# Kernel tuning notes

Measured on AMD Instinct MI355X. Metric: run time of the kernel, lower is better.

The kernel has to match this reference:

```python
import jax, jax.numpy as jnp
import numpy as np

V, E, T, H, Z = 32000, 512, 64, 1024, 128
B = 64
PAD = 31999


def _lin(x, W, b):
    return x @ W.T + b


def _lstm_cell(x, h, c, Wih, Whh, bih, bhh):
    gates = x @ Wih.T + bih + h @ Whh.T + bhh  # [B,4H], torch gate order i,f,g,o
    i, f, g, o = jnp.split(gates, 4, axis=-1)
    c = jax.nn.sigmoid(f) * c + jax.nn.sigmoid(i) * jnp.tanh(g)
    h = jax.nn.sigmoid(o) * jnp.tanh(c)
    return h, c


def _forward(enc_input, dec_input, length, eps, enc_emb, enc_Wih, enc_Whh, enc_bih, enc_bhh,
             latent_W, latent_b, dec_emb, attn_W, attn_b, combine_W, combine_b,
             dec_Wih, dec_Whh, dec_bih, dec_bhh, pri_W, pri_b, inf_W, inf_b,
             aux_W, aux_b, out_W, out_b):
    # All lengths == T, so the descending sort and pack/pad are identity ops.
    att_mask = enc_input == PAD  # [B,T]
    x_enc = enc_emb[enc_input]   # [B,T,E]

    def enc_step(carry, x):
        h, c = carry
        h, c = _lstm_cell(x, h, c, enc_Wih, enc_Whh, enc_bih, enc_bhh)
        return (h, c), h

    h0 = jnp.zeros((B, H), x_enc.dtype)
    (h_T, c_T), enc_out = jax.lax.scan(enc_step, (h0, h0), jnp.swapaxes(x_enc, 0, 1))
    enc_output = jnp.swapaxes(enc_out, 0, 1)  # [B,T,H]

    mu, logvar = jnp.split(_lin(jnp.concatenate([h_T, c_T], -1), latent_W, latent_b), 2, -1)
    z = mu + jnp.exp(0.5 * logvar) * eps  # [B,Z]

    x_dec = dec_emb[dec_input]  # [B,T+1,E]; dropout off (eval mode)

    def dec_step(carry, inp):
        h, c = carry
        x, t = inp
        pri_mu, pri_lv = jnp.split(_lin(h, pri_W, pri_b), 2, -1)
        scale = _lin(jnp.concatenate([x, h], -1), attn_W, attn_b)  # [B,T]
        scale = jnp.where(att_mask, -jnp.inf, scale)
        attn_w = jax.nn.softmax(scale, -1)
        context = jnp.einsum('bt,bth->bh', attn_w, enc_output)
        inf_mu, inf_lv = jnp.split(_lin(jnp.concatenate([h, context], -1), inf_W, inf_b), 2, -1)
        mask = (length + 1 > t).astype(x.dtype)  # [B]
        kld = 0.5 * jnp.sum(pri_lv - inf_lv + jnp.exp(inf_lv - pri_lv)
                            + (inf_mu - pri_mu) ** 2 / jnp.exp(pri_lv) - 1.0, axis=1) * mask
        z_step = pri_mu  # eval mode (torch: reparameterize(inf_mu, inf_lv) when training)
        aux_mu = _lin(z_step, aux_W, aux_b)
        aux_c = jnp.sum((jax.lax.stop_gradient(context) - aux_mu) ** 2, axis=1)
        u = _lin(jnp.concatenate([x, aux_mu, z_step, z], -1), combine_W, combine_b)
        h, c = _lstm_cell(u, h, c, dec_Wih, dec_Whh, dec_bih, dec_bhh)
        return (h, c), (h, kld, aux_c)

    ts = jnp.arange(T + 1)
    _, (hs, klds, aux_cs) = jax.lax.scan(dec_step, (h0, h0), (jnp.swapaxes(x_dec, 0, 1), ts))
    output = jnp.swapaxes(hs, 0, 1)  # [B,T+1,H]

    logit = output @ out_W.T + out_b  # [B,T+1,V]
    logp = jax.nn.log_softmax(logit, -1)
    return logp, mu, logvar, jnp.sum(klds), jnp.sum(aux_cs)


def setup_inputs() -> dict:
    key = jax.random.key(0)
    ks = jax.random.split(key, 32)
    s = 0.02
    d = {
        'enc_input': jax.random.randint(ks[0], (B, T), 0, V - 1),
        'dec_input': jax.random.randint(ks[1], (B, T + 1), 0, V - 1),
        'length': jnp.full((B,), T, dtype=jnp.int32),
        'eps': jax.random.normal(ks[2], (B, Z), jnp.float32),
        'enc_emb': (jax.random.normal(ks[3], (V, E)) * s).at[PAD].set(0.0),
        'enc_Wih': jax.random.normal(ks[4], (4 * H, E)) * s,
        'enc_Whh': jax.random.normal(ks[5], (4 * H, H)) * s,
        'enc_bih': jax.random.normal(ks[6], (4 * H,)) * s,
        'enc_bhh': jax.random.normal(ks[7], (4 * H,)) * s,
        'latent_W': jax.random.normal(ks[8], (2 * Z, 2 * H)) * s,
        'latent_b': jax.random.normal(ks[9], (2 * Z,)) * s,
        'dec_emb': (jax.random.normal(ks[10], (V, E)) * s).at[PAD].set(0.0),
        'attn_W': jax.random.normal(ks[11], (T, H + E)) * s,
        'attn_b': jax.random.normal(ks[12], (T,)) * s,
        'combine_W': jax.random.normal(ks[13], (H, H + E + 2 * Z)) * s,
        'combine_b': jax.random.normal(ks[14], (H,)) * s,
        'dec_Wih': jax.random.normal(ks[15], (4 * H, H)) * s,
        'dec_Whh': jax.random.normal(ks[16], (4 * H, H)) * s,
        'dec_bih': jax.random.normal(ks[17], (4 * H,)) * s,
        'dec_bhh': jax.random.normal(ks[18], (4 * H,)) * s,
        'pri_W': jax.random.normal(ks[19], (2 * Z, H)) * s,
        'pri_b': jax.random.normal(ks[20], (2 * Z,)) * s,
        'inf_W': jax.random.normal(ks[21], (2 * Z, 2 * H)) * s,
        'inf_b': jax.random.normal(ks[22], (2 * Z,)) * s,
        'aux_W': jax.random.normal(ks[23], (H, Z)) * s,
        'aux_b': jax.random.normal(ks[24], (H,)) * s,
        'out_W': jax.random.normal(ks[25], (V, H)) * s,
        'out_b': jax.random.normal(ks[26], (V,)) * s,
    }
    return d


def reference(enc_input, dec_input, length, eps, enc_emb, enc_Wih, enc_Whh, enc_bih, enc_bhh,
              latent_W, latent_b, dec_emb, attn_W, attn_b, combine_W, combine_b,
              dec_Wih, dec_Whh, dec_bih, dec_bhh, pri_W, pri_b, inf_W, inf_b,
              aux_W, aux_b, out_W, out_b):
    return _forward(enc_input, dec_input, length, eps, enc_emb, enc_Wih, enc_Whh, enc_bih,
                    enc_bhh, latent_W, latent_b, dec_emb, attn_W, attn_b, combine_W, combine_b,
                    dec_Wih, dec_Whh, dec_bih, dec_bhh, pri_W, pri_b, inf_W, inf_b,
                    aux_W, aux_b, out_W, out_b)
```

## Files before the change

kernel.cpp:

```cpp
#include <hip/hip_runtime.h>
#include <hip/hip_bf16.h>
#include <cmath>

typedef unsigned short u16;
typedef __attribute__((ext_vector_type(8))) short short8;
typedef __attribute__((ext_vector_type(4))) float floatx4;

#define DEVI __device__ __forceinline__

constexpr int cV = 32000, cE = 512, cT = 64, cH = 1024, cZ = 128, cB = 64, cPAD = 31999, cTP1 = 65;
constexpr long long LOGP_SZ = 133120000LL;
constexpr long long AMAT_OFF = 130990080LL;
constexpr long long WBOUT_OFF = 38400000LL;
constexpr int SKIP_LO = 1200, SKIP_HI = 1712;

DEVI float b2f(u16 u) { return __uint_as_float(((unsigned)u) << 16); }
DEVI u16 f2b(float f) {
  unsigned u = __float_as_uint(f);
  unsigned r = u + 0x7FFFu + ((u >> 16) & 1u);
  return (u16)(r >> 16);
}
DEVI unsigned pk2(float lo, float hi) {
  __hip_bfloat162 t = __float22bfloat162_rn(make_float2(lo, hi));
  return *reinterpret_cast<unsigned*>(&t);
}
DEVI float sigm(float x) { return 1.f / (1.f + expf(-x)); }

DEVI short8 ldfragW(const float* __restrict__ p) {
  float4 x = *(const float4*)p, y = *(const float4*)(p + 4);
  union { unsigned u[4]; short8 s; } r;
  r.u[0] = pk2(x.x, x.y); r.u[1] = pk2(x.z, x.w);
  r.u[2] = pk2(y.x, y.y); r.u[3] = pk2(y.z, y.w);
  return r.s;
}

template <typename T>
DEVI short8 ldfrag(const T* __restrict__ p) {
  if constexpr (sizeof(T) == 2) return *(const short8*)(p);
  else return ldfragW((const float*)p);
}

template <int MAP>
DEVI int rmap(int r) {
  if constexpr (MAP == 1) return ((r & 3) << 10) | (r >> 2);
  else if constexpr (MAP == 2) return r & 63;
  else return r;
}

DEVI float dot_wf(const float* __restrict__ w, const float* __restrict__ s, int K) {
  float a0 = 0.f, a1 = 0.f, a2 = 0.f, a3 = 0.f;
#pragma unroll 4
  for (int k = 0; k < K; k += 8) {
    float4 p = *(const float4*)(w + k);
    float4 q = *(const float4*)(w + k + 4);
    a0 = fmaf(s[k + 0], p.x, a0); a1 = fmaf(s[k + 1], p.y, a1);
    a2 = fmaf(s[k + 2], p.z, a2); a3 = fmaf(s[k + 3], p.w, a3);
    a0 = fmaf(s[k + 4], q.x, a0); a1 = fmaf(s[k + 5], q.y, a1);
    a2 = fmaf(s[k + 6], q.z, a2); a3 = fmaf(s[k + 7], q.w, a3);
  }
  return (a0 + a1) + (a2 + a3);
}

__global__ __launch_bounds__(256) void k_zero(float* p, int n) {
  int i = blockIdx.x * 256 + threadIdx.x;
  if (i < n) p[i] = 0.f;
}

template <typename AT, typename BT, typename CT, int AMAP, int BMAP, bool ADDC>
__global__ __launch_bounds__(64) void k_gemm(
    const AT* __restrict__ A, int lda, const BT* __restrict__ B, int ldb,
    const float* __restrict__ bias, const float* __restrict__ Dm, int ldd,
    CT* __restrict__ C, int ldc, int K) {
  int nblk = blockIdx.x, mblk = blockIdx.y;
  int lane = threadIdx.x;
  int lr = lane & 15, kg = lane >> 4;
  const BT* Bp = B + (size_t)rmap<BMAP>(nblk * 16 + lr) * ldb + kg * 8;
  const AT* Ap[4];
#pragma unroll
  for (int mf = 0; mf < 4; mf++)
    Ap[mf] = A + (size_t)rmap<AMAP>(mblk * 64 + mf * 16 + lr) * lda + kg * 8;
  floatx4 acc[4];
#pragma unroll
  for (int mf = 0; mf < 4; mf++) acc[mf] = (floatx4){0.f, 0.f, 0.f, 0.f};
#pragma unroll 4
  for (int ks = 0; ks < K / 32; ks++) {
    short8 bv = ldfrag(Bp + ks * 32);
#pragma unroll
    for (int mf = 0; mf < 4; mf++) {
      short8 av = ldfrag(Ap[mf] + ks * 32);
      acc[mf] = __builtin_amdgcn_mfma_f32_16x16x32_bf16(av, bv, acc[mf], 0, 0, 0);
    }
  }
  int n = nblk * 16 + lr;
  float bs = bias ? bias[n] : 0.f;
#pragma unroll
  for (int mf = 0; mf < 4; mf++) {
#pragma unroll
    for (int jj = 0; jj < 4; jj++) {
      int m = mblk * 64 + mf * 16 + kg * 4 + jj;
      size_t ci = (size_t)m * ldc + n;
      float v = acc[mf][jj] + bs;
      if (Dm) v += Dm[(size_t)rmap<AMAP>(m) * ldd + n];
      if constexpr (ADDC) {
        if constexpr (sizeof(CT) == 2) v += b2f(C[ci]);
        else v += C[ci];
      }
      if constexpr (sizeof(CT) == 2) C[ci] = f2b(v);
      else C[ci] = v;
    }
  }
}

__global__ __launch_bounds__(64) void k_cell2(
    const u16* __restrict__ G, const u16* __restrict__ H, int strideH,
    const u16* __restrict__ Wb, float* __restrict__ c,
    u16* __restrict__ out1, int s1, u16* __restrict__ Afrag, int t) {
  int nb = blockIdx.x;
  int lane = threadIdx.x;
  int lr = lane & 15, kg = lane >> 4;
  const u16* Bp = Wb + (size_t)(nb * 16 + lr) * cH + kg * 8;
  floatx4 acc[4];
#pragma unroll
  for (int mf = 0; mf < 4; mf++) acc[mf] = (floatx4){0.f, 0.f, 0.f, 0.f};
#pragma unroll 8
  for (int ks = 0; ks < 32; ks++) {
    short8 bv = *(const short8*)(Bp + ks * 32);
#pragma unroll
    for (int mf = 0; mf < 4; mf++) {
      short8 av = *(const short8*)(H + (size_t)(mf * 16 + lr) * strideH + ks * 32 + kg * 8);
      acc[mf] = __builtin_amdgcn_mfma_f32_16x16x32_bf16(av, bv, acc[mf], 0, 0, 0);
    }
  }
  __shared__ float lds[16][65];
#pragma unroll
  for (int mf = 0; mf < 4; mf++)
#pragma unroll
    for (int jj = 0; jj < 4; jj++)
      lds[lr][mf * 16 + kg * 4 + jj] = acc[mf][jj];
  __syncthreads();
#pragma unroll
  for (int a = 0; a < 4; a++) {
    int b = lane;
    int j = nb * 4 + a;
    ushort4 gv = *(const ushort4*)(G + (size_t)b * 4096 + nb * 16 + 4 * a);
    float gi = lds[4 * a + 0][b] + b2f(gv.x);
    float gf = lds[4 * a + 1][b] + b2f(gv.y);
    float gg = lds[4 * a + 2][b] + b2f(gv.z);
    float go = lds[4 * a + 3][b] + b2f(gv.w);
    int ci = b * cH + j;
    float cc = c[ci];
    cc = sigm(gf) * cc + sigm(gi) * tanhf(gg);
    float hh = sigm(go) * tanhf(cc);
    c[ci] = cc;
    u16 hb = f2b(hh);
    out1[(size_t)b * s1 + j] = hb;
    if (Afrag) {
      int m = b * cTP1 + t;
      size_t idx = ((size_t)(m >> 4) * 32 + (j >> 5)) * 512 +
                   ((((j >> 3) & 3) * 16) + (m & 15)) * 8 + (j & 7);
      Afrag[idx] = hb;
    }
  }
}

__global__ __launch_bounds__(256) void k_tr(const float* __restrict__ src, int ld,
                                            int R, float* __restrict__ dst) {
  __shared__ float tile[32][33];
  int c0 = blockIdx.x * 32, r0 = blockIdx.y * 32;
  int tx = threadIdx.x & 31, ty = threadIdx.x >> 5;
  for (int i = ty; i < 32; i += 8) tile[i][tx] = src[(size_t)(r0 + i) * ld + c0 + tx];
  __syncthreads();
  for (int i = ty; i < 32; i += 8) dst[(size_t)(c0 + i) * R + r0 + tx] = tile[tx][i];
}

__global__ __launch_bounds__(256) void k_gemv(const float* __restrict__ W, int ld,
                                              const float* __restrict__ x,
                                              const float* __restrict__ b,
                                              float* __restrict__ out, int K, int add) {
  int n = blockIdx.x * 256 + threadIdx.x;
  const float* w = W + (size_t)n * ld;
  float s = b ? b[n] : 0.f;
  for (int k = 0; k < K; k += 4) {
    float4 wv = *(const float4*)(w + k);
    float4 xv = *(const float4*)(x + k);
    s += wv.x * xv.x + wv.y * xv.y + wv.z * xv.z + wv.w * xv.w;
  }
  if (add) out[n] += s; else out[n] = s;
}

__global__ __launch_bounds__(256) void k_biasD(const float* __restrict__ bih,
                                               const float* __restrict__ bhh,
                                               const float* __restrict__ Wih,
                                               const float* __restrict__ u0,
                                               float* __restrict__ biasD) {
  int np = blockIdx.x * 256 + threadIdx.x;
  int src = ((np & 3) << 10) | (np >> 2);
  const float* w = Wih + (size_t)src * cH;
  float s = bih[src] + bhh[src];
  for (int k = 0; k < cH; k += 4) {
    float4 wv = *(const float4*)(w + k);
    float4 xv = *(const float4*)(u0 + k);
    s += wv.x * xv.x + wv.y * xv.y + wv.z * xv.z + wv.w * xv.w;
  }
  biasD[np] = s;
}

__global__ __launch_bounds__(256) void k_biasE(const float* __restrict__ bih,
                                               const float* __restrict__ bhh,
                                               float* __restrict__ biasE) {
  int np = blockIdx.x * 256 + threadIdx.x;
  int src = ((np & 3) << 10) | (np >> 2);
  biasE[np] = bih[src] + bhh[src];
}

__global__ __launch_bounds__(256) void k_permW(const float* __restrict__ Whh,
                                               u16* __restrict__ Wp) {
  int np = blockIdx.x;
  int src = ((np & 3) << 10) | (np >> 2);
  const float* w = Whh + (size_t)src * cH;
  u16* d = Wp + (size_t)np * cH;
  int tid = threadIdx.x;
#pragma unroll
  for (int p = 0; p < 4; p++) d[tid + p * 256] = f2b(w[tid + p * 256]);
}

__global__ __launch_bounds__(256) void k_cvtW(const float* __restrict__ W,
                                              u16* __restrict__ Wf) {
  int g = blockIdx.x * 4 + (threadIdx.x >> 6);
  int l = threadIdx.x & 63;
  int nblk = g >> 5, kb = g & 31;
  const float* src = W + (size_t)(nblk * 16 + (l & 15)) * cH + kb * 32 + (l >> 4) * 8;
  *(short8*)(Wf + (size_t)g * 512 + l * 8) = ldfragW(src);
}

__global__ __launch_bounds__(256) void k_gather(const int* __restrict__ tok,
                                                const float* __restrict__ emb,
                                                u16* __restrict__ dst, int Tlen) {
  int r = blockIdx.x;
  int t = r >> 6, b = r & 63;
  const float* src = emb + (size_t)tok[b * Tlen + t] * cE;
  u16* d = dst + (size_t)r * cE;
  int tid = threadIdx.x;
  for (int k = tid; k < cE; k += 256) d[k] = f2b(src[k]);
}

__global__ __launch_bounds__(256) void k_latent(
    const u16* __restrict__ encO, const float* __restrict__ cT2,
    const float* __restrict__ W, const float* __restrict__ bias,
    float* __restrict__ mulv, float* __restrict__ outp) {
  __shared__ float s[2 * cH];
  int b = blockIdx.x;
  int n = threadIdx.x;
  for (int k = n; k < cH; k += 256) {
    s[k] = b2f(encO[((size_t)b * cT + 63) * cH + k]);
    s[cH + k] = cT2[b * cH + k];
  }
  __syncthreads();
  float acc = bias[n] + dot_wf(W + (size_t)n * (2 * cH), s, 2 * cH);
  mulv[b * 256 + n] = acc;
  if (n < cZ)
    outp[LOGP_SZ + (size_t)b * cZ + n] = acc;
  else
    outp[LOGP_SZ + (size_t)cB * cZ + (size_t)b * cZ + (n - cZ)] = acc;
}

__global__ __launch_bounds__(256) void k_z(const float* __restrict__ mulv,
                                           const float* __restrict__ eps,
                                           u16* __restrict__ zbuf) {
  int i = blockIdx.x * 256 + threadIdx.x;
  if (i >= cB * cZ) return;
  int b = i >> 7, zi = i & 127;
  float mu = mulv[b * 256 + zi], lv = mulv[b * 256 + cZ + zi];
  zbuf[i] = f2b(mu + expf(0.5f * lv) * eps[i]);
}

__global__ __launch_bounds__(256) void k_sctx(
    const float* __restrict__ S, const int* __restrict__ enc_input,
    const u16* __restrict__ encO, u16* __restrict__ ctxH) {
  __shared__ float wat[cT];
  int tb = blockIdx.x;
  int b = tb & 63;
  int tid = threadIdx.x;
  if (tid < cT) {
    float sc = S[(size_t)tb * cT + tid];
    if (enc_input[b * cT + tid] == cPAD) sc = -INFINITY;
    float m = sc;
#pragma unroll
    for (int off = 32; off >= 1; off >>= 1) m = fmaxf(m, __shfl_xor(m, off));
    float p = expf(sc - m);
    float ssum = p;
#pragma unroll
    for (int off = 32; off >= 1; off >>= 1) ssum += __shfl_xor(ssum, off);
    wat[tid] = p / ssum;
  }
  __syncthreads();
#pragma unroll
  for (int p = 0; p < 4; p++) {
    int j = tid + p * 256;
    float s = 0.f;
    const u16* e = encO + ((size_t)b * cT) * cH + j;
#pragma unroll 8
    for (int t2 = 0; t2 < cT; t2++) s += wat[t2] * b2f(e[(size_t)t2 * cH]);
    ctxH[(size_t)tb * cH + j] = f2b(s);
  }
}

__global__ __launch_bounds__(256) void k_scal_all(
    const float* __restrict__ priH, const float* __restrict__ infH,
    const u16* __restrict__ ctxH, const u16* __restrict__ auxH,
    const int* __restrict__ length, float* __restrict__ scal) {
  __shared__ float red[256];
  int tb = blockIdx.x;
  int t = tb >> 6, b = tb & 63;
  int tid = threadIdx.x;
  float r = 0.f;
  if (tid < cZ) {
    float pm = priH[(size_t)tb * 256 + tid], plv = priH[(size_t)tb * 256 + cZ + tid];
    float im = infH[(size_t)tb * 256 + tid], ilv = infH[(size_t)tb * 256 + cZ + tid];
    float d = im - pm;
    r = plv - ilv + expf(ilv - plv) + d * d * expf(-plv) - 1.f;
  }
  red[tid] = r;
  __syncthreads();
  for (int sft = 128; sft > 0; sft >>= 1) {
    if (tid < sft) red[tid] += red[tid + sft];
    __syncthreads();
  }
  if (tid == 0 && (length[b] + 1 > t)) atomicAdd(&scal[0], 0.5f * red[0]);
  __syncthreads();
  float r2 = 0.f;
#pragma unroll
  for (int p = 0; p < 4; p++) {
    int j = tid + p * 256;
    float d = b2f(ctxH[(size_t)tb * cH + j]) - b2f(auxH[(size_t)tb * cH + j]);
    r2 += d * d;
  }
  red[tid] = r2;
  __syncthreads();
  for (int sft = 128; sft > 0; sft >>= 1) {
    if (tid < sft) red[tid] += red[tid + sft];
    __syncthreads();
  }
  if (tid == 0) atomicAdd(&scal[1], red[0]);
}

__global__ void k_scal(const float* __restrict__ scal, float* __restrict__ outp) {
  if (threadIdx.x == 0) {
    outp[LOGP_SZ + 2 * cB * cZ] = scal[0];
    outp[LOGP_SZ + 2 * cB * cZ + 1] = scal[1];
  }
}

__global__ __launch_bounds__(256) void k_cpyA(const u16* __restrict__ src,
                                              u16* __restrict__ dst) {
  int i = blockIdx.x * 256 + threadIdx.x;
  ((uint4*)dst)[i] = ((const uint4*)(src + (size_t)252 * 32 * 512))[i];
}

template <bool WFRAG>
__global__ __launch_bounds__(512) void k_logit3(
    const u16* __restrict__ Af, int fragBase,
    const u16* __restrict__ Wf, const float* __restrict__ Wraw,
    const float* __restrict__ bias, float* __restrict__ outp,
    int mStart, int mEnd, int storeLo, int storeHi, int skipLo, int skipHi) {
  __shared__ u16 wpan[32768];
  int nb = blockIdx.x;
  int tid = threadIdx.x;
  if constexpr (WFRAG) {
    const uint4* src = (const uint4*)(Wf + (size_t)nb * 32768);
    uint4* dst = (uint4*)wpan;
#pragma unroll
    for (int q = 0; q < 8; q++) dst[tid + q * 512] = src[tid + q * 512];
  } else {
    int wv = tid >> 6, l = tid & 63;
    for (int f = wv; f < 64; f += 8) {
      int fr = f >> 5, kb = f & 31;
      const float* src = Wraw + (size_t)(nb * 32 + fr * 16 + (l & 15)) * cH + kb * 32 + (l >> 4) * 8;
      *(short8*)(wpan + f * 512 + l * 8) = ldfragW(src);
    }
  }
  __syncthreads();
  int wave = tid >> 6, lane = tid & 63;
  int lr = lane & 15, kg = lane >> 4;
  for (int m0 = mStart; m0 < mEnd; m0 += 512) {
    int mi = m0 + wave * 64;
    int mfg[4];
#pragma unroll
    for (int mf = 0; mf < 4; mf++) {
      int g = (mi >> 4) + mf;
      if (g > 259) g = 259;
      mfg[mf] = g - fragBase;
    }
    floatx4 acc[4][2];
#pragma unroll
    for (int mf = 0; mf < 4; mf++)
#pragma unroll
      for (int ni = 0; ni < 2; ni++) acc[mf][ni] = (floatx4){0.f, 0.f, 0.f, 0.f};
#pragma unroll 4
    for (int ks = 0; ks < 32; ks++) {
      short8 bv0 = *(const short8*)(wpan + ks * 512 + lane * 8);
      short8 bv1 = *(const short8*)(wpan + (32 + ks) * 512 + lane * 8);
#pragma unroll
      for (int mf = 0; mf < 4; mf++) {
        short8 av = *(const short8*)(Af + ((size_t)mfg[mf] * 32 + ks) * 512 + lane * 8);
        acc[mf][0] = __builtin_amdgcn_mfma_f32_16x16x32_bf16(av, bv0, acc[mf][0], 0, 0, 0);
        acc[mf][1] = __builtin_amdgcn_mfma_f32_16x16x32_bf16(av, bv1, acc[mf][1], 0, 0, 0);
      }
    }
#pragma unroll
    for (int mf = 0; mf < 4; mf++) {
#pragma unroll
      for (int ni = 0; ni < 2; ni++) {
        int n = nb * 32 + ni * 16 + lr;
        float bb = bias[n];
#pragma unroll
        for (int jj = 0; jj < 4; jj++) {
          int m = mi + mf * 16 + kg * 4 + jj;
          if (m >= storeLo && m < storeHi && !(m >= skipLo && m < skipHi))
            outp[(size_t)m * cV + n] = acc[mf][ni][jj] + bb;
        }
      }
    }
  }
}

__global__ __launch_bounds__(256) void k_lsm(float* __restrict__ outp) {
  __shared__ float wm_[4], ws_[4];
  __shared__ float blz;
  int m = blockIdx.x;
  int tid = threadIdx.x, lane = tid & 63, wid = tid >> 6;
  float4* rp4 = (float4*)(outp + (size_t)m * cV);
  float mx = -INFINITY, sm = 0.f;
  for (int n = tid; n < cV / 4; n += 256) {
    float4 v = rp4[n];
    float lm = fmaxf(fmaxf(v.x, v.y), fmaxf(v.z, v.w));
    float nm = fmaxf(mx, lm);
    sm = sm * expf(mx - nm) + expf(v.x - nm) + expf(v.y - nm) + expf(v.z - nm) + expf(v.w - nm);
    mx = nm;
  }
#pragma unroll
  for (int off = 32; off >= 1; off >>= 1) {
    float om = __shfl_xor(mx, off), os = __shfl_xor(sm, off);
    float nm = fmaxf(mx, om);
    sm = sm * expf(mx - nm) + os * expf(om - nm);
    mx = nm;
  }
  if (lane == 0) { wm_[wid] = mx; ws_[wid] = sm; }
  __syncthreads();
  if (tid == 0) {
    float M = fmaxf(fmaxf(wm_[0], wm_[1]), fmaxf(wm_[2], wm_[3]));
    float S = ws_[0] * expf(wm_[0] - M) + ws_[1] * expf(wm_[1] - M) +
              ws_[2] * expf(wm_[2] - M) + ws_[3] * expf(wm_[3] - M);
    blz = M + logf(S);
  }
  __syncthreads();
  float lz = blz;
  for (int n = tid; n < cV / 4; n += 256) {
    float4 v = rp4[n];
    v.x -= lz; v.y -= lz; v.z -= lz; v.w -= lz;
    rp4[n] = v;
  }
}

extern "C" void kernel_launch(void* const* d_in, const int* in_sizes, int n_in,
                              void* d_out, int out_size, void* d_ws, size_t ws_size,
                              hipStream_t stream) {
  (void)in_sizes; (void)n_in; (void)out_size; (void)ws_size;
  const int* enc_input  = (const int*)d_in[0];
  const int* dec_input  = (const int*)d_in[1];
  const int* length     = (const int*)d_in[2];
  const float* eps      = (const float*)d_in[3];
  const float* enc_emb  = (const float*)d_in[4];
  const float* enc_Wih  = (const float*)d_in[5];
  const float* enc_Whh  = (const float*)d_in[6];
  const float* enc_bih  = (const float*)d_in[7];
  const float* enc_bhh  = (const float*)d_in[8];
  const float* latent_W = (const float*)d_in[9];
  const float* latent_b = (const float*)d_in[10];
  const float* dec_emb  = (const float*)d_in[11];
  const float* attn_W   = (const float*)d_in[12];
  const float* attn_b   = (const float*)d_in[13];
  const float* comb_W   = (const float*)d_in[14];
  const float* comb_b   = (const float*)d_in[15];
  const float* dec_Wih  = (const float*)d_in[16];
  const float* dec_Whh  = (const float*)d_in[17];
  const float* dec_bih  = (const float*)d_in[18];
  const float* dec_bhh  = (const float*)d_in[19];
  const float* pri_W    = (const float*)d_in[20];
  const float* pri_b    = (const float*)d_in[21];
  const float* inf_W    = (const float*)d_in[22];
  const float* inf_b    = (const float*)d_in[23];
  const float* aux_W    = (const float*)d_in[24];
  const float* aux_b    = (const float*)d_in[25];
  const float* out_W    = (const float*)d_in[26];
  const float* out_b    = (const float*)d_in[27];
  float* outp = (float*)d_out;
  float* outF = outp;

  size_t off = 0;
  float* c_enc = outF + off; off += 65536;
  float* c_dec = outF + off; off += 65536;
  float* scal  = outF + off; off += 4;
  off += 60;
  u16* HencZ = (u16*)(outF + off); off += 32768;
  u16* Hh    = (u16*)(outF + off); off += 66 * 32768;
  size_t zeroSpan = 196672;
  u16* encO  = (u16*)(outF + off); off += 2097152;
  u16* Xenc  = (u16*)(outF + off); off += 1048576;
  u16* Xdec  = (u16*)(outF + off); off += 1064960;
  u16* zbuf  = (u16*)(outF + off); off += 4096;
  float* mulv  = outF + off; off += 16384;
  float* biasE = outF + off; off += 4096;
  float* biasD = outF + off; off += 4096;
  float* tmp1  = outF + off; off += 1024;
  float* u0    = outF + off; off += 1024;
  float* WcxT  = outF + off; off += 524288;
  float* WczT  = outF + off; off += 131072;
  float* wPmT  = outF + off; off += 131072;
  float* auxWT = outF + off; off += 131072;
  float* M1    = outF + off; off += 131072;
  float* WfT   = outF + off; off += 1048576;
  u16* WhhEp = (u16*)(outF + off); off += 2097152;
  u16* Wbig  = (u16*)(outF + off); off += 2097152;
  u16* C1    = (u16*)(outF + off); off += 1048576;
  u16* C2    = (u16*)(outF + off); off += 262144;
  u16* Genc  = (u16*)(outF + off); off += 8388608;
  u16* Gdec  = (u16*)(outF + off); off += 8519680;
  float* priH = outF + off; off += 1064960;
  float* infH = outF + off; off += 1064960;
  float* S    = outF + off; off += 266240;
  u16* ctxH  = (u16*)(outF + off); off += 2129920;
  u16* auxH  = (u16*)(outF + off); off += 2129920;
  u16* Wf   = (u16*)(outF + WBOUT_OFF);
  u16* Amat = (u16*)(outF + AMAT_OFF);
  u16* wsA = (u16*)d_ws;

  k_cvtW<<<16000, 256, 0, stream>>>(out_W, Wf);
  k_tr<<<dim3(16, 32), 256, 0, stream>>>(comb_W, 1792, 1024, WcxT);
  k_tr<<<dim3(4, 32), 256, 0, stream>>>(comb_W + 1664, 1792, 1024, WczT);
  k_tr<<<dim3(32, 4), 256, 0, stream>>>(pri_W, 1024, 128, wPmT);
  k_tr<<<dim3(4, 32), 256, 0, stream>>>(aux_W, 128, 1024, auxWT);
  k_gemv<<<4, 256, 0, stream>>>(aux_W, 128, pri_b, aux_b, tmp1, 128, 0);
  k_gemv<<<4, 256, 0, stream>>>(comb_W + 512, 1792, tmp1, comb_b, u0, 1024, 0);
  k_gemv<<<4, 256, 0, stream>>>(comb_W + 1536, 1792, pri_b, nullptr, u0, 128, 1);
  k_biasE<<<16, 256, 0, stream>>>(enc_bih, enc_bhh, biasE);
  k_biasD<<<16, 256, 0, stream>>>(dec_bih, dec_bhh, dec_Wih, u0, biasD);
  k_permW<<<4096, 256, 0, stream>>>(enc_Whh, WhhEp);
  k_gather<<<cT * cB, 256, 0, stream>>>(enc_input, enc_emb, Xenc, cT);
  k_gather<<<cTP1 * cB, 256, 0, stream>>>(dec_input, dec_emb, Xdec, cTP1);
  k_zero<<<(int)((zeroSpan + 255) / 256), 256, 0, stream>>>(c_enc, (int)zeroSpan);

  k_gemm<float, float, float, 0, 0, false><<<dim3(8, 16), 64, 0, stream>>>(
      comb_W + 512, 1792, auxWT, 1024, nullptr, comb_W + 1536, 1792, M1, 128, 1024);
  k_gemm<float, float, float, 0, 0, false><<<dim3(64, 16), 64, 0, stream>>>(
      wPmT, 128, M1, 128, nullptr, nullptr, 0, WfT, 1024, 128);
  k_gemm<float, float, u16, 1, 0, false><<<dim3(64, 64), 64, 0, stream>>>(
      dec_Wih, 1024, WfT, 1024, nullptr, dec_Whh, 1024, Wbig, 1024, 1024);
  k_gemm<float, float, u16, 1, 0, false><<<dim3(32, 64), 64, 0, stream>>>(
      dec_Wih, 1024, WcxT, 1024, nullptr, nullptr, 0, C1, 512, 1024);
  k_gemm<float, float, u16, 1, 0, false><<<dim3(8, 64), 64, 0, stream>>>(
      dec_Wih, 1024, WczT, 1024, nullptr, nullptr, 0, C2, 128, 1024);
  k_gemm<u16, float, u16, 0, 1, false><<<dim3(256, 64), 64, 0, stream>>>(
      Xenc, 512, enc_Wih, 512, biasE, nullptr, 0, Genc, 4096, 512);

  for (int t = 0; t < cT; t++) {
    const u16* Hcur = t ? (encO + (size_t)(t - 1) * cH) : HencZ;
    int sH = t ? (cT * cH) : cH;
    k_cell2<<<256, 64, 0, stream>>>(Genc + (size_t)t * cB * 4096, Hcur, sH, WhhEp,
                                    c_enc, encO + (size_t)t * cH, cT * cH, nullptr, 0);
  }
  k_latent<<<cB, 256, 0, stream>>>(encO, c_enc, latent_W, latent_b, mulv, outp);
  k_z<<<(cB * cZ + 255) / 256, 256, 0, stream>>>(mulv, eps, zbuf);

  k_gemm<u16, u16, u16, 0, 0, false><<<dim3(256, 65), 64, 0, stream>>>(
      Xdec, 512, C1, 512, biasD, nullptr, 0, Gdec, 4096, 512);
  k_gemm<u16, u16, u16, 2, 0, true><<<dim3(256, 65), 64, 0, stream>>>(
      zbuf, 128, C2, 128, nullptr, nullptr, 0, Gdec, 4096, 128);

  for (int t = 0; t < cTP1; t++) {
    k_cell2<<<256, 64, 0, stream>>>(Gdec + (size_t)t * cB * 4096,
                                    Hh + (size_t)t * cB * cH, cH, Wbig, c_dec,
                                    Hh + (size_t)(t + 1) * cB * cH, cH,
                                    Amat, t);
  }

  k_gemm<u16, float, float, 0, 0, false><<<dim3(16, 65), 64, 0, stream>>>(
      Hh, 1024, pri_W, 1024, pri_b, nullptr, 0, priH, 256, 1024);
  k_gemm<u16, float, float, 0, 0, false><<<dim3(4, 65), 64, 0, stream>>>(
      Xdec, 512, attn_W, 1536, attn_b, nullptr, 0, S, 64, 512);
  k_gemm<u16, float, float, 0, 0, true><<<dim3(4, 65), 64, 0, stream>>>(
      Hh, 1024, attn_W + 512, 1536, nullptr, nullptr, 0, S, 64, 1024);
  k_sctx<<<cTP1 * cB, 256, 0, stream>>>(S, enc_input, encO, ctxH);
  k_gemm<u16, float, float, 0, 0, false><<<dim3(16, 65), 64, 0, stream>>>(
      Hh, 1024, inf_W, 2048, inf_b, nullptr, 0, infH, 256, 1024);
  k_gemm<u16, float, float, 0, 0, true><<<dim3(16, 65), 64, 0, stream>>>(
      ctxH, 1024, inf_W + 1024, 2048, nullptr, nullptr, 0, infH, 256, 1024);
  k_gemm<float, float, u16, 0, 0, false><<<dim3(64, 65), 64, 0, stream>>>(
      priH, 256, aux_W, 128, aux_b, nullptr, 0, auxH, 1024, 128);
  k_scal_all<<<cTP1 * cB, 256, 0, stream>>>(priH, infH, ctxH, auxH, length, scal);
  k_scal<<<1, 64, 0, stream>>>(scal, outp);

  k_cpyA<<<32, 256, 0, stream>>>(Amat, wsA);
  k_logit3<true><<<1000, 512, 0, stream>>>(Amat, 0, Wf, nullptr, out_b, outp,
                                           0, 4096, 0, 4093, SKIP_LO, SKIP_HI);
  k_logit3<false><<<1000, 512, 0, stream>>>(Amat, 0, nullptr, out_W, out_b, outp,
                                            SKIP_LO, SKIP_HI, SKIP_LO, SKIP_HI, 0, 0);
  k_logit3<false><<<1000, 512, 0, stream>>>(wsA, 252, nullptr, out_W, out_b, outp,
                                            4032, 4160, 4093, 4160, 0, 0);
  k_lsm<<<cB * cTP1, 256, 0, stream>>>(outp);
}
```

Before: 4.017 ms.

## Run LSTM recurrences as persistent cooperative kernels and widen logit tiles

Replaces the per-timestep k_cell2 launches for the encoder and decoder with one persistent cooperative kernel each. Each block caches its recurrent-weight panel in LDS, keeps the cell state in registers, and uses grid.sync between timesteps, removing per-step launch overhead and repeated weight reloads. The output-logit kernel is also widened to 64 vocab columns per block (500 blocks), doubling LDS weight reuse per A-fragment load. Risks are grid-sync latency on 256 blocks, a 128KB LDS panel per logit block that limits occupancy, and a Wf fragment layout that must match the new 64-column blocking.

```diff
diff --git a/kernel.cpp b/kernel.cpp
--- a/kernel.cpp
+++ b/kernel.cpp
@@ -1,6 +1,9 @@
 #include <hip/hip_runtime.h>
 #include <hip/hip_bf16.h>
+#include <hip/hip_cooperative_groups.h>
 #include <cmath>
+
+namespace cg = cooperative_groups;
 
 typedef unsigned short u16;
 typedef __attribute__((ext_vector_type(8))) short short8;
@@ -111,55 +114,83 @@
   }
 }
 
-__global__ __launch_bounds__(64) void k_cell2(
-    const u16* __restrict__ G, const u16* __restrict__ H, int strideH,
-    const u16* __restrict__ Wb, float* __restrict__ c,
-    u16* __restrict__ out1, int s1, u16* __restrict__ Afrag, int t) {
+template <int NSTEPS, bool DEC>
+__global__ __launch_bounds__(64) void k_cells_all(
+    const u16* __restrict__ G,
+    const u16* __restrict__ H0,
+    const u16* __restrict__ Wb,
+    u16* __restrict__ Hist,
+    u16* __restrict__ Afrag) {
+  cg::grid_group grid = cg::this_grid();
   int nb = blockIdx.x;
   int lane = threadIdx.x;
   int lr = lane & 15, kg = lane >> 4;
-  const u16* Bp = Wb + (size_t)(nb * 16 + lr) * cH + kg * 8;
-  floatx4 acc[4];
-#pragma unroll
-  for (int mf = 0; mf < 4; mf++) acc[mf] = (floatx4){0.f, 0.f, 0.f, 0.f};
+  __shared__ u16 wpan[16384];
+  __shared__ float ldsT[16][65];
+  {
+    const u16* src = Wb + (size_t)(nb * 16 + lr) * cH + kg * 8;
+#pragma unroll 4
+    for (int ks = 0; ks < 32; ks++)
+      *(short8*)(wpan + ks * 512 + lane * 8) = *(const short8*)(src + ks * 32);
+  }
+  float creg[4] = {0.f, 0.f, 0.f, 0.f};
+  __syncthreads();
+  for (int t = 0; t < NSTEPS; t++) {
+    const u16* H;
+    int strideH;
+    if constexpr (DEC) {
+      H = Hist + (size_t)t * cB * cH; strideH = cH;
+    } else {
+      H = t ? (Hist + (size_t)(t - 1) * cH) : H0;
+      strideH = t ? (cT * cH) : cH;
+    }
+    floatx4 acc[4];
+#pragma unroll
+    for (int mf = 0; mf < 4; mf++) acc[mf] = (floatx4){0.f, 0.f, 0.f, 0.f};
 #pragma unroll 8
-  for (int ks = 0; ks < 32; ks++) {
-    short8 bv = *(const short8*)(Bp + ks * 32);
-#pragma unroll
-    for (int mf = 0; mf < 4; mf++) {
-      short8 av = *(const short8*)(H + (size_t)(mf * 16 + lr) * strideH + ks * 32 + kg * 8);
-      acc[mf] = __builtin_amdgcn_mfma_f32_16x16x32_bf16(av, bv, acc[mf], 0, 0, 0);
-    }
-  }
-  __shared__ float lds[16][65];
-#pragma unroll
-  for (int mf = 0; mf < 4; mf++)
-#pragma unroll
-    for (int jj = 0; jj < 4; jj++)
-      lds[lr][mf * 16 + kg * 4 + jj] = acc[mf][jj];
-  __syncthreads();
-#pragma unroll
-  for (int a = 0; a < 4; a++) {
+    for (int ks = 0; ks < 32; ks++) {
+      short8 bv = *(const short8*)(wpan + ks * 512 + lane * 8);
+#pragma unroll
+      for (int mf = 0; mf < 4; mf++) {
+        short8 av = *(const short8*)(H + (size_t)(mf * 16 + lr) * strideH + ks * 32 + kg * 8);
+        acc[mf] = __builtin_amdgcn_mfma_f32_16x16x32_bf16(av, bv, acc[mf], 0, 0, 0);
+      }
+    }
+#pragma unroll
+    for (int mf = 0; mf < 4; mf++)
+#pragma unroll
+      for (int jj = 0; jj < 4; jj++)
+        ldsT[lr][mf * 16 + kg * 4 + jj] = acc[mf][jj];
+    __syncthreads();
     int b = lane;
-    int j = nb * 4 + a;
-    ushort4 gv = *(const ushort4*)(G + (size_t)b * 4096 + nb * 16 + 4 * a);
-    float gi = lds[4 * a + 0][b] + b2f(gv.x);
-    float gf = lds[4 * a + 1][b] + b2f(gv.y);
-    float gg = lds[4 * a + 2][b] + b2f(gv.z);
-    float go = lds[4 * a + 3][b] + b2f(gv.w);
-    int ci = b * cH + j;
-    float cc = c[ci];
-    cc = sigm(gf) * cc + sigm(gi) * tanhf(gg);
-    float hh = sigm(go) * tanhf(cc);
-    c[ci] = cc;
-    u16 hb = f2b(hh);
-    out1[(size_t)b * s1 + j] = hb;
-    if (Afrag) {
+    const u16* gp = G + ((size_t)t * cB + b) * 4096 + nb * 16;
+    u16 hb[4];
+#pragma unroll
+    for (int a = 0; a < 4; a++) {
+      ushort4 gv = *(const ushort4*)(gp + 4 * a);
+      float gi = ldsT[4 * a + 0][b] + b2f(gv.x);
+      float gf = ldsT[4 * a + 1][b] + b2f(gv.y);
+      float gg = ldsT[4 * a + 2][b] + b2f(gv.z);
+      float go = ldsT[4 * a + 3][b] + b2f(gv.w);
+      float cc = creg[a];
+      cc = sigm(gf) * cc + sigm(gi) * tanhf(gg);
+      float hh = sigm(go) * tanhf(cc);
+      creg[a] = cc;
+      hb[a] = f2b(hh);
+    }
+    ushort4 hv = {hb[0], hb[1], hb[2], hb[3]};
+    int j0 = nb * 4;
+    if constexpr (DEC) {
+      *(ushort4*)(Hist + ((size_t)(t + 1) * cB + b) * cH + j0) = hv;
       int m = b * cTP1 + t;
-      size_t idx = ((size_t)(m >> 4) * 32 + (j >> 5)) * 512 +
-                   ((((j >> 3) & 3) * 16) + (m & 15)) * 8 + (j & 7);
-      Afrag[idx] = hb;
-    }
+      size_t aidx = ((size_t)(m >> 4) * 32 + (j0 >> 5)) * 512 +
+                    (size_t)((((j0 >> 3) & 3) * 16 + (m & 15)) * 8 + (j0 & 7));
+      *(ushort4*)(Afrag + aidx) = hv;
+    } else {
+      *(ushort4*)(Hist + (size_t)b * (cT * cH) + (size_t)t * cH + j0) = hv;
+    }
+    __syncthreads();
+    grid.sync();
   }
 }
 
@@ -263,6 +294,7 @@
   else
     outp[LOGP_SZ + (size_t)cB * cZ + (size_t)b * cZ + (n - cZ)] = acc;
 }
+
 
 __global__ __launch_bounds__(256) void k_z(const float* __restrict__ mulv,
                                            const float* __restrict__ eps,
@@ -358,25 +390,25 @@
 }
 
 template <bool WFRAG>
-__global__ __launch_bounds__(512) void k_logit3(
+__global__ __launch_bounds__(512) void k_logit5(
     const u16* __restrict__ Af, int fragBase,
     const u16* __restrict__ Wf, const float* __restrict__ Wraw,
     const float* __restrict__ bias, float* __restrict__ outp,
     int mStart, int mEnd, int storeLo, int storeHi, int skipLo, int skipHi) {
-  __shared__ u16 wpan[32768];
+  __shared__ u16 wpan[65536];
   int nb = blockIdx.x;
   int tid = threadIdx.x;
   if constexpr (WFRAG) {
-    const uint4* src = (const uint4*)(Wf + (size_t)nb * 32768);
+    const uint4* src = (const uint4*)(Wf + (size_t)nb * 65536);
     uint4* dst = (uint4*)wpan;
 #pragma unroll
-    for (int q = 0; q < 8; q++) dst[tid + q * 512] = src[tid + q * 512];
+    for (int q = 0; q < 16; q++) dst[tid + q * 512] = src[tid + q * 512];
   } else {
     int wv = tid >> 6, l = tid & 63;
-    for (int f = wv; f < 64; f += 8) {
+    for (int f = wv; f < 128; f += 8) {
       int fr = f >> 5, kb = f & 31;
-      const float* src = Wraw + (size_t)(nb * 32 + fr * 16 + (l & 15)) * cH + kb * 32 + (l >> 4) * 8;
-      *(short8*)(wpan + f * 512 + l * 8) = ldfragW(src);
+      const float* src = Wraw + (size_t)(nb * 64 + fr * 16 + (l & 15)) * cH + kb * 32 + (l >> 4) * 8;
+      *(short8*)(wpan + (size_t)f * 512 + l * 8) = ldfragW(src);
     }
   }
   __syncthreads();
@@ -391,33 +423,36 @@
       if (g > 259) g = 259;
       mfg[mf] = g - fragBase;
     }
-    floatx4 acc[4][2];
+    floatx4 acc[4][4];
 #pragma unroll
     for (int mf = 0; mf < 4; mf++)
 #pragma unroll
-      for (int ni = 0; ni < 2; ni++) acc[mf][ni] = (floatx4){0.f, 0.f, 0.f, 0.f};
-#pragma unroll 4
+      for (int fr = 0; fr < 4; fr++) acc[mf][fr] = (floatx4){0.f, 0.f, 0.f, 0.f};
+#pragma unroll 2
     for (int ks = 0; ks < 32; ks++) {
-      short8 bv0 = *(const short8*)(wpan + ks * 512 + lane * 8);
-      short8 bv1 = *(const short8*)(wpan + (32 + ks) * 512 + lane * 8);
+      short8 bv[4];
+#pragma unroll
+      for (int fr = 0; fr < 4; fr++)
+        bv[fr] = *(const short8*)(wpan + ((size_t)(fr * 32 + ks) * 512) + lane * 8);
 #pragma unroll
       for (int mf = 0; mf < 4; mf++) {
         short8 av = *(const short8*)(Af + ((size_t)mfg[mf] * 32 + ks) * 512 + lane * 8);
-        acc[mf][0] = __builtin_amdgcn_mfma_f32_16x16x32_bf16(av, bv0, acc[mf][0], 0, 0, 0);
-        acc[mf][1] = __builtin_amdgcn_mfma_f32_16x16x32_bf16(av, bv1, acc[mf][1], 0, 0, 0);
+#pragma unroll
+        for (int fr = 0; fr < 4; fr++)
+          acc[mf][fr] = __builtin_amdgcn_mfma_f32_16x16x32_bf16(av, bv[fr], acc[mf][fr], 0, 0, 0);
       }
     }
 #pragma unroll
     for (int mf = 0; mf < 4; mf++) {
 #pragma unroll
-      for (int ni = 0; ni < 2; ni++) {
-        int n = nb * 32 + ni * 16 + lr;
+      for (int fr = 0; fr < 4; fr++) {
+        int n = nb * 64 + fr * 16 + lr;
         float bb = bias[n];
 #pragma unroll
         for (int jj = 0; jj < 4; jj++) {
           int m = mi + mf * 16 + kg * 4 + jj;
           if (m >= storeLo && m < storeHi && !(m >= skipLo && m < skipHi))
-            outp[(size_t)m * cV + n] = acc[mf][ni][jj] + bb;
+            outp[(size_t)m * cV + n] = acc[mf][fr][jj] + bb;
         }
       }
     }
@@ -459,6 +494,73 @@
     float4 v = rp4[n];
     v.x -= lz; v.y -= lz; v.z -= lz; v.w -= lz;
     rp4[n] = v;
+  }
+}
+
+template <int NSTEPS>
+__global__ __launch_bounds__(64) void k_cells_enc(
+    const u16* __restrict__ G, const u16* __restrict__ H0,
+    const u16* __restrict__ Wb, u16* __restrict__ Hist,
+    float* __restrict__ cOut) {
+  cg::grid_group grid = cg::this_grid();
+  int nb = blockIdx.x;
+  int lane = threadIdx.x;
+  int lr = lane & 15, kg = lane >> 4;
+  __shared__ u16 wpan[16384];
+  __shared__ float ldsT[16][65];
+  {
+    const u16* src = Wb + (size_t)(nb * 16 + lr) * cH + kg * 8;
+#pragma unroll 4
+    for (int ks = 0; ks < 32; ks++)
+      *(short8*)(wpan + ks * 512 + lane * 8) = *(const short8*)(src + ks * 32);
+  }
+  float creg[4] = {0.f, 0.f, 0.f, 0.f};
+  __syncthreads();
+  for (int t = 0; t < NSTEPS; t++) {
+    const u16* H = t ? (Hist + (size_t)(t - 1) * cH) : H0;
+    int strideH = t ? (cT * cH) : cH;
+    floatx4 acc[4];
+#pragma unroll
+    for (int mf = 0; mf < 4; mf++) acc[mf] = (floatx4){0.f, 0.f, 0.f, 0.f};
+#pragma unroll 8
+    for (int ks = 0; ks < 32; ks++) {
+      short8 bv = *(const short8*)(wpan + ks * 512 + lane * 8);
+#pragma unroll
+      for (int mf = 0; mf < 4; mf++) {
+        short8 av = *(const short8*)(H + (size_t)(mf * 16 + lr) * strideH + ks * 32 + kg * 8);
+        acc[mf] = __builtin_amdgcn_mfma_f32_16x16x32_bf16(av, bv, acc[mf], 0, 0, 0);
+      }
+    }
+#pragma unroll
+    for (int mf = 0; mf < 4; mf++)
+#pragma unroll
+      for (int jj = 0; jj < 4; jj++)
+        ldsT[lr][mf * 16 + kg * 4 + jj] = acc[mf][jj];
+    __syncthreads();
+    int b = lane;
+    const u16* gp = G + ((size_t)t * cB + b) * 4096 + nb * 16;
+    u16 hb[4];
+#pragma unroll
+    for (int a = 0; a < 4; a++) {
+      ushort4 gv = *(const ushort4*)(gp + 4 * a);
+      float gi = ldsT[4 * a + 0][b] + b2f(gv.x);
+      float gf = ldsT[4 * a + 1][b] + b2f(gv.y);
+      float gg = ldsT[4 * a + 2][b] + b2f(gv.z);
+      float go = ldsT[4 * a + 3][b] + b2f(gv.w);
+      float cc = creg[a];
+      cc = sigm(gf) * cc + sigm(gi) * tanhf(gg);
+      float hh = sigm(go) * tanhf(cc);
+      creg[a] = cc;
+      hb[a] = f2b(hh);
+    }
+    ushort4 hv = {hb[0], hb[1], hb[2], hb[3]};
+    int j0 = nb * 4;
+    *(ushort4*)(Hist + (size_t)b * (cT * cH) + (size_t)t * cH + j0) = hv;
+    if (t == NSTEPS - 1)
+      *(float4*)(cOut + (size_t)b * cH + j0) =
+          make_float4(creg[0], creg[1], creg[2], creg[3]);
+    __syncthreads();
+    grid.sync();
   }
 }
 
@@ -563,11 +665,11 @@
   k_gemm<u16, float, u16, 0, 1, false><<<dim3(256, 64), 64, 0, stream>>>(
       Xenc, 512, enc_Wih, 512, biasE, nullptr, 0, Genc, 4096, 512);
 
-  for (int t = 0; t < cT; t++) {
-    const u16* Hcur = t ? (encO + (size_t)(t - 1) * cH) : HencZ;
-    int sH = t ? (cT * cH) : cH;
-    k_cell2<<<256, 64, 0, stream>>>(Genc + (size_t)t * cB * 4096, Hcur, sH, WhhEp,
-                                    c_enc, encO + (size_t)t * cH, cT * cH, nullptr, 0);
+  {
+    void (*fn)(const u16*, const u16*, const u16*, u16*, float*) = k_cells_enc<cT>;
+    void* args[] = {(void*)&Genc, (void*)&HencZ, (void*)&WhhEp, (void*)&encO, (void*)&c_enc};
+    hipLaunchCooperativeKernel(reinterpret_cast<void*>(fn), dim3(256), dim3(64),
+                               args, 0, stream);
   }
   k_latent<<<cB, 256, 0, stream>>>(encO, c_enc, latent_W, latent_b, mulv, outp);
   k_z<<<(cB * cZ + 255) / 256, 256, 0, stream>>>(mulv, eps, zbuf);
@@ -577,11 +679,12 @@
   k_gemm<u16, u16, u16, 2, 0, true><<<dim3(256, 65), 64, 0, stream>>>(
       zbuf, 128, C2, 128, nullptr, nullptr, 0, Gdec, 4096, 128);
 
-  for (int t = 0; t < cTP1; t++) {
-    k_cell2<<<256, 64, 0, stream>>>(Gdec + (size_t)t * cB * 4096,
-                                    Hh + (size_t)t * cB * cH, cH, Wbig, c_dec,
-                                    Hh + (size_t)(t + 1) * cB * cH, cH,
-                                    Amat, t);
+  {
+    void (*fn)(const u16*, const u16*, const u16*, u16*, u16*) = k_cells_all<cTP1, true>;
+    u16* nullH = nullptr;
+    void* args[] = {(void*)&Gdec, (void*)&nullH, (void*)&Wbig, (void*)&Hh, (void*)&Amat};
+    hipLaunchCooperativeKernel(reinterpret_cast<void*>(fn), dim3(256), dim3(64),
+                               args, 0, stream);
   }
 
   k_gemm<u16, float, float, 0, 0, false><<<dim3(16, 65), 64, 0, stream>>>(
@@ -601,11 +704,11 @@
   k_scal<<<1, 64, 0, stream>>>(scal, outp);
 
   k_cpyA<<<32, 256, 0, stream>>>(Amat, wsA);
-  k_logit3<true><<<1000, 512, 0, stream>>>(Amat, 0, Wf, nullptr, out_b, outp,
-                                           0, 4096, 0, 4093, SKIP_LO, SKIP_HI);
-  k_logit3<false><<<1000, 512, 0, stream>>>(Amat, 0, nullptr, out_W, out_b, outp,
-                                            SKIP_LO, SKIP_HI, SKIP_LO, SKIP_HI, 0, 0);
-  k_logit3<false><<<1000, 512, 0, stream>>>(wsA, 252, nullptr, out_W, out_b, outp,
-                                            4032, 4160, 4093, 4160, 0, 0);
+  k_logit5<true><<<500, 512, 0, stream>>>(Amat, 0, Wf, nullptr, out_b, outp,
+                                          0, 4096, 0, 4093, SKIP_LO, SKIP_HI);
+  k_logit5<false><<<500, 512, 0, stream>>>(Amat, 0, nullptr, out_W, out_b, outp,
+                                           SKIP_LO, SKIP_HI, SKIP_LO, SKIP_HI, 0, 0);
+  k_logit5<false><<<500, 512, 0, stream>>>(wsA, 252, nullptr, out_W, out_b, outp,
+                                           4032, 4160, 4093, 4160, 0, 0);
   k_lsm<<<cB * cTP1, 256, 0, stream>>>(outp);
 }
```

Result: slower. 7.618 ms (+89.6%).
